# Optimization experiments

Hardware: AMD Instinct MI355X
Metric: run time of the kernel (lower is better)

## Reference

```python
import jax, jax.numpy as jnp
import numpy as np

N, E, FDIM, HID, HEADS, C, L, G = 50000, 800000, 512, 256, 8, 32, 3, 64
EPS = 1e-5


def setup_inputs() -> dict:
    key = jax.random.key(0)
    ks = jax.random.split(key, 16)
    x = jax.random.normal(ks[0], (N, FDIM), dtype=jnp.float32)
    edge_index = jax.random.randint(ks[1], (2, E), 0, N, dtype=jnp.int32)
    batch = jnp.sort(jax.random.randint(ks[2], (N,), 0, G, dtype=jnp.int32))
    s = lambda f: 1.0 / np.sqrt(f)
    return {
        "x": x,
        "edge_index": edge_index,
        "batch": batch,
        "in_w": jax.random.normal(ks[3], (FDIM, HID), jnp.float32) * s(FDIM),
        "in_b": jnp.zeros((HID,), jnp.float32),
        "gat_w": jax.random.normal(ks[4], (L, HID, HID), jnp.float32) * s(HID),
        "att_src": jax.random.normal(ks[5], (L, HEADS, C), jnp.float32) * s(C),
        "att_dst": jax.random.normal(ks[6], (L, HEADS, C), jnp.float32) * s(C),
        "gat_b": jnp.zeros((L, HID), jnp.float32),
        "res_w": jax.random.normal(ks[7], (L, HID, HID), jnp.float32) * s(HID),
        "res_b": jnp.zeros((L, HID), jnp.float32),
        "ln_g": jnp.ones((L, HID), jnp.float32),
        "ln_b": jnp.zeros((L, HID), jnp.float32),
        "pool_w": jax.random.normal(ks[8], (2 * HID, HID), jnp.float32) * s(2 * HID),
        "pool_b": jnp.zeros((HID,), jnp.float32),
    }


def _gat_layer(h, src, dst, w, a_src, a_dst, b):
    # PyG GATConv, concat=True, negative_slope=0.2, dropout inactive (eval)
    xh = (h @ w).reshape(N, HEADS, C)                      # [N,H,C]
    asn = jnp.einsum('nhc,hc->nh', xh, a_src)              # [N,H]
    adn = jnp.einsum('nhc,hc->nh', xh, a_dst)
    e = jax.nn.leaky_relu(asn[src] + adn[dst], 0.2)        # [E2,H]
    # scatter-softmax over destination neighborhoods
    m = jax.ops.segment_max(e, dst, num_segments=N)
    m = jnp.where(jnp.isfinite(m), m, 0.0)
    ex = jnp.exp(e - m[dst])
    den = jax.ops.segment_sum(ex, dst, num_segments=N)
    alpha = ex / (den[dst] + 1e-16)                        # [E2,H]
    msg = xh[src] * alpha[:, :, None]                      # [E2,H,C]
    out = jax.ops.segment_sum(msg, dst, num_segments=N)    # [N,H,C]
    return out.reshape(N, HID) + b


def _layer_norm(h, g, b):
    mu = jnp.mean(h, axis=-1, keepdims=True)
    var = jnp.mean((h - mu) ** 2, axis=-1, keepdims=True)
    return (h - mu) * jax.lax.rsqrt(var + EPS) * g + b


def reference(x, edge_index, batch, in_w, in_b, gat_w, att_src, att_dst, gat_b,
              res_w, res_b, ln_g, ln_b, pool_w, pool_b):
    loops = jnp.arange(N, dtype=edge_index.dtype)          # GATConv add_self_loops=True
    src = jnp.concatenate([edge_index[0], loops])
    dst = jnp.concatenate([edge_index[1], loops])
    h = x @ in_w + in_b
    for i in range(L):
        h_res = h @ res_w[i] + res_b[i]
        h = _gat_layer(h, src, dst, gat_w[i], att_src[i], att_dst[i], gat_b[i])
        h = jax.nn.relu(_layer_norm(h + h_res, ln_g[i], ln_b[i]))
    ones = jnp.ones((N,), h.dtype)
    cnt = jax.ops.segment_sum(ones, batch, num_segments=G)
    h_mean = jax.ops.segment_sum(h, batch, num_segments=G) / jnp.maximum(cnt, 1.0)[:, None]
    h_max = jax.ops.segment_max(h, batch, num_segments=G)
    h_cat = jnp.concatenate([h_mean, h_max], axis=1)       # [G, 2*HID]
    return jax.nn.relu(h_cat @ pool_w + pool_b)            # [G, HID]
```

## Files before the change

kernel.cpp:

```cpp
#include <hip/hip_runtime.h>
#include <math.h>

#define N_NODES 50000
#define E_EDGES 800000
#define E2 (E_EDGES + N_NODES)
#define M_PAD 50048
#define FDIM 512
#define HID 256
#define HEADS 8
#define CDIM 32
#define LAYERS 3
#define GRAPHS 64
#define LN_EPS 1e-5f
#define POOL_P 16

typedef unsigned short ushort_t;
typedef __attribute__((ext_vector_type(8))) short short8v;
typedef __attribute__((ext_vector_type(4))) float f32x4;

__device__ __forceinline__ float bf2f(ushort_t u) {
    union { unsigned int i; float f; } v;
    v.i = ((unsigned int)u) << 16;
    return v.f;
}
__device__ __forceinline__ ushort_t f2bf(float f) {
    union { float f; unsigned int u; } v;
    v.f = f;
    unsigned int r = (v.u + 0x7FFFu + ((v.u >> 16) & 1u)) >> 16;
    return (ushort_t)r;
}
__device__ __forceinline__ void gload_lds16(const void* g, void* l) {
    __builtin_amdgcn_global_load_lds(
        (const __attribute__((address_space(1))) void*)g,
        (__attribute__((address_space(3))) void*)l, 16, 0, 0);
}

__global__ void k_count(const int* __restrict__ ei, int* __restrict__ cnt) {
    int e = blockIdx.x * 256 + threadIdx.x;
    if (e >= E2) return;
    int dst = (e < E_EDGES) ? ei[E_EDGES + e] : (e - E_EDGES);
    atomicAdd(&cnt[dst], 1);
}

__global__ void k_scan1(const int* __restrict__ cnt, int* __restrict__ part) {
    __shared__ int s[256];
    int t = threadIdx.x;
    int i = blockIdx.x * 256 + t;
    s[t] = (i < N_NODES) ? cnt[i] : 0;
    __syncthreads();
    for (int d = 128; d > 0; d >>= 1) {
        if (t < d) s[t] += s[t + d];
        __syncthreads();
    }
    if (t == 0) part[blockIdx.x] = s[0];
}

__global__ void k_scan2(int* __restrict__ part, int nb, int* __restrict__ rowptr) {
    __shared__ int s[256];
    int t = threadIdx.x;
    int v = (t < nb) ? part[t] : 0;
    s[t] = v;
    __syncthreads();
    for (int d = 1; d < 256; d <<= 1) {
        int x = (t >= d) ? s[t - d] : 0;
        __syncthreads();
        s[t] += x;
        __syncthreads();
    }
    if (t < nb) part[t] = s[t] - v;
    if (t == 255) rowptr[N_NODES] = s[255];
}

__global__ void k_scan3(const int* __restrict__ cnt, const int* __restrict__ part,
                        int* __restrict__ rowptr) {
    __shared__ int s[256];
    int t = threadIdx.x;
    int i = blockIdx.x * 256 + t;
    int v = (i < N_NODES) ? cnt[i] : 0;
    s[t] = v;
    __syncthreads();
    for (int d = 1; d < 256; d <<= 1) {
        int x = (t >= d) ? s[t - d] : 0;
        __syncthreads();
        s[t] += x;
        __syncthreads();
    }
    if (i < N_NODES) rowptr[i] = part[blockIdx.x] + s[t] - v;
}

__global__ void k_fill(const int* __restrict__ ei, const int* __restrict__ rowptr,
                       int* __restrict__ fill, int* __restrict__ colv) {
    int e = blockIdx.x * 256 + threadIdx.x;
    if (e >= E2) return;
    int src, dst;
    if (e < E_EDGES) { src = ei[e]; dst = ei[E_EDGES + e]; }
    else             { src = dst = e - E_EDGES; }
    int pos = atomicAdd(&fill[dst], 1);
    colv[rowptr[dst] + pos] = src;
}

__global__ void k_bounds(const int* __restrict__ batch, int* __restrict__ rowstart) {
    int n = blockIdx.x * 256 + threadIdx.x;
    if (n >= N_NODES) return;
    int b = batch[n];
    int bp = (n == 0) ? -1 : batch[n - 1];
    for (int g = bp + 1; g <= b; ++g) rowstart[g] = n;
    if (n == N_NODES - 1) {
        for (int g = b + 1; g <= GRAPHS; ++g) rowstart[g] = N_NODES;
    }
}

__global__ __launch_bounds__(256) void k_cast_x(const float* __restrict__ x,
                                                ushort_t* __restrict__ xb) {
    long long i8 = ((long long)blockIdx.x * 256 + threadIdx.x) * 8;
    if (i8 >= (long long)M_PAD * FDIM) return;
    int row = (int)(i8 >> 9);
    ushort_t o[8];
    if (row < N_NODES) {
        const float* p = x + i8;
        #pragma unroll
        for (int j = 0; j < 8; ++j) o[j] = f2bf(p[j]);
    } else {
        #pragma unroll
        for (int j = 0; j < 8; ++j) o[j] = 0;
    }
    *(short8v*)(xb + i8) = *(short8v*)o;
}

#define IN_ELEMS (FDIM * HID)
#define MAT_ELEMS (HID * HID)
#define WT_TOTAL (IN_ELEMS + 2 * LAYERS * MAT_ELEMS)
__global__ __launch_bounds__(256) void k_wtrans_all(const float* __restrict__ in_w,
                                                    const float* __restrict__ gat_w,
                                                    const float* __restrict__ res_w,
                                                    ushort_t* __restrict__ wt_in,
                                                    ushort_t* __restrict__ wt2) {
    int id = blockIdx.x * 256 + threadIdx.x;
    if (id >= WT_TOTAL) return;
    if (id < IN_ELEMS) {
        int k = id >> 8, n = id & 255;
        wt_in[(size_t)n * FDIM + k] = f2bf(in_w[id]);
    } else {
        int r = id - IN_ELEMS;
        int mat = r >> 16;
        int layer = mat >> 1;
        int isgat = mat & 1;
        int within = r & 65535;
        int k = within >> 8, n = within & 255;
        const float* W = (isgat ? gat_w : res_w) + (size_t)layer * MAT_ELEMS;
        wt2[(size_t)layer * 512 * HID + (size_t)(isgat * 256 + n) * HID + k] =
            f2bf(W[within]);
    }
}

template<int K>
__global__ __launch_bounds__(256) void k_gemm_bf16(const ushort_t* __restrict__ A,
                                                   const ushort_t* __restrict__ BT,
                                                   const float* __restrict__ bias0,
                                                   const float* __restrict__ bias1,
                                                   ushort_t* __restrict__ C0,
                                                   ushort_t* __restrict__ C1, int M) {
    __shared__ char lds[16384] __attribute__((aligned(16)));
    const int bm = blockIdx.x * 128;
    const int bn = blockIdx.y * 128;
    const int t = threadIdx.x, w = t >> 6, l = t & 63;
    const int wr = w >> 1, wc = w & 1;

    const int c1 = t, c2 = t + 256;
    const int ar1 = c1 >> 2, as1 = (c1 & 3) ^ ((ar1 >> 1) & 3);
    const int ar2 = c2 >> 2, as2 = (c2 & 3) ^ ((ar2 >> 1) & 3);
    const ushort_t* pa1 = A + (size_t)(bm + ar1) * K + as1 * 8;
    const ushort_t* pa2 = A + (size_t)(bm + ar2) * K + as2 * 8;
    const ushort_t* pb1 = BT + (size_t)(bn + ar1) * K + as1 * 8;
    const ushort_t* pb2 = BT + (size_t)(bn + ar2) * K + as2 * 8;
    char* la1 = lds + w * 1024;
    char* la2 = lds + 4096 + w * 1024;
    char* lb1 = lds + 8192 + w * 1024;
    char* lb2 = lds + 12288 + w * 1024;

    int aoff[4], boff[4];
    const int kb = l >> 4;
    #pragma unroll
    for (int mi = 0; mi < 4; ++mi) {
        int r = wr * 64 + mi * 16 + (l & 15);
        aoff[mi] = r * 64 + ((kb ^ ((r >> 1) & 3)) << 4);
        int c = wc * 64 + mi * 16 + (l & 15);
        boff[mi] = 8192 + c * 64 + ((kb ^ ((c >> 1) & 3)) << 4);
    }

    f32x4 acc[4][4] = {};
    for (int k0 = 0; k0 < K; k0 += 32) {
        gload_lds16(pa1 + k0, la1);
        gload_lds16(pa2 + k0, la2);
        gload_lds16(pb1 + k0, lb1);
        gload_lds16(pb2 + k0, lb2);
        __syncthreads();
        short8v a[4], b[4];
        #pragma unroll
        for (int mi = 0; mi < 4; ++mi) a[mi] = *(const short8v*)(lds + aoff[mi]);
        #pragma unroll
        for (int ni = 0; ni < 4; ++ni) b[ni] = *(const short8v*)(lds + boff[ni]);
        #pragma unroll
        for (int mi = 0; mi < 4; ++mi)
            #pragma unroll
            for (int ni = 0; ni < 4; ++ni)
                acc[mi][ni] = __builtin_amdgcn_mfma_f32_16x16x32_bf16(
                    a[mi], b[ni], acc[mi][ni], 0, 0, 0);
        __syncthreads();
    }

    ushort_t* C = (bn < 256) ? C0 : C1;
    const float* bias = (bn < 256) ? bias0 : bias1;
    const int cb = (bn < 256) ? bn : bn - 256;
    #pragma unroll
    for (int mi = 0; mi < 4; ++mi) {
        int row = bm + wr * 64 + mi * 16 + (l >> 4) * 4;
        #pragma unroll
        for (int ni = 0; ni < 4; ++ni) {
            int col = cb + wc * 64 + ni * 16 + (l & 15);
            float bv = bias ? bias[col] : 0.f;
            #pragma unroll
            for (int r = 0; r < 4; ++r) {
                if (row + r < M)
                    C[(size_t)(row + r) * HID + col] = f2bf(acc[mi][ni][r] + bv);
            }
        }
    }
}

__global__ __launch_bounds__(256) void k_scores(const ushort_t* __restrict__ xhb,
                                                const float* __restrict__ a_src,
                                                const float* __restrict__ a_dst,
                                                float* __restrict__ asn,
                                                float* __restrict__ adn) {
    int wave = threadIdx.x >> 6, lane = threadIdx.x & 63;
    int n = blockIdx.x * 4 + wave;
    if (n >= N_NODES) return;
    int head = lane >> 3, part = lane & 7;
    ushort4 u = *(const ushort4*)(xhb + (size_t)n * HID + head * CDIM + part * 4);
    float vx = bf2f(u.x), vy = bf2f(u.y), vz = bf2f(u.z), vw = bf2f(u.w);
    const float4 ws = *(const float4*)(a_src + head * CDIM + part * 4);
    const float4 wd = *(const float4*)(a_dst + head * CDIM + part * 4);
    float ds_ = vx * ws.x + vy * ws.y + vz * ws.z + vw * ws.w;
    float dd_ = vx * wd.x + vy * wd.y + vz * wd.z + vw * wd.w;
    for (int d = 1; d < 8; d <<= 1) {
        ds_ += __shfl_xor(ds_, d);
        dd_ += __shfl_xor(dd_, d);
    }
    if (part == 0) {
        asn[n * HEADS + head] = ds_;
        adn[n * HEADS + head] = dd_;
    }
}

__global__ __launch_bounds__(256) void k_agg_ln(const ushort_t* __restrict__ xhb,
                                                const float* __restrict__ asn,
                                                const float* __restrict__ adn,
                                                const int* __restrict__ rowptr,
                                                const int* __restrict__ colv,
                                                const ushort_t* __restrict__ hresb,
                                                const float* __restrict__ gb,
                                                const float* __restrict__ g,
                                                const float* __restrict__ b,
                                                ushort_t* __restrict__ hb) {
    const int wave = threadIdx.x >> 6, lane = threadIdx.x & 63;
    const int n = blockIdx.x * 4 + wave;
    if (n >= N_NODES) return;
    const int half = lane >> 5;
    const int lh = lane & 31;
    const int head = lh >> 2;
    const int ch0 = lh * 8;
    const float adn_h = adn[n * HEADS + head];
    const int j0 = rowptr[n], j1 = rowptr[n + 1];

    float acc[8] = {};
    float den = 0.f;
    int base = j0;
    for (; base + 8 <= j1; base += 8) {
        int idx[4];
        #pragma unroll
        for (int q = 0; q < 4; ++q) idx[q] = colv[base + 2 * q + half];
        short8v u[4];
        #pragma unroll
        for (int q = 0; q < 4; ++q)
            u[q] = *(const short8v*)(xhb + (size_t)idx[q] * HID + ch0);
        float p[4];
        #pragma unroll
        for (int q = 0; q < 4; ++q) {
            float e = asn[idx[q] * HEADS + head] + adn_h;
            e = (e > 0.f) ? e : 0.2f * e;
            p[q] = __expf(e);
        }
        #pragma unroll
        for (int q = 0; q < 4; ++q) {
            den += p[q];
            #pragma unroll
            for (int c = 0; c < 8; ++c)
                acc[c] += p[q] * bf2f((ushort_t)u[q][c]);
        }
    }
    for (; base < j1; base += 2) {
        bool valid = (base + half) < j1;
        int s = valid ? colv[base + half] : n;
        short8v u = *(const short8v*)(xhb + (size_t)s * HID + ch0);
        float e = asn[s * HEADS + head] + adn_h;
        e = (e > 0.f) ? e : 0.2f * e;
        float p = valid ? __expf(e) : 0.f;
        den += p;
        #pragma unroll
        for (int c = 0; c < 8; ++c)
            acc[c] += p * bf2f((ushort_t)u[c]);
    }
    den += __shfl_xor(den, 32);
    #pragma unroll
    for (int c = 0; c < 8; ++c) acc[c] += __shfl_xor(acc[c], 32);

    const float inv = 1.f / (den + 1e-16f);
    short8v hr = *(const short8v*)(hresb + (size_t)n * HID + ch0);
    float4 gbA = *(const float4*)(gb + ch0);
    float4 gbB = *(const float4*)(gb + ch0 + 4);
    float v[8];
    #pragma unroll
    for (int c = 0; c < 8; ++c) {
        float gbv = (c < 4) ? ((const float*)&gbA)[c] : ((const float*)&gbB)[c - 4];
        v[c] = acc[c] * inv + bf2f((ushort_t)hr[c]) + gbv;
    }
    float s = 0.f;
    #pragma unroll
    for (int c = 0; c < 8; ++c) s += v[c];
    #pragma unroll
    for (int d = 1; d < 32; d <<= 1) s += __shfl_xor(s, d);
    const float mu = s * (1.f / HID);
    float q = 0.f;
    #pragma unroll
    for (int c = 0; c < 8; ++c) {
        v[c] -= mu;
        q += v[c] * v[c];
    }
    #pragma unroll
    for (int d = 1; d < 32; d <<= 1) q += __shfl_xor(q, d);
    const float rstd = rsqrtf(q * (1.f / HID) + LN_EPS);
    float4 gA = *(const float4*)(g + ch0);
    float4 gB = *(const float4*)(g + ch0 + 4);
    float4 bA = *(const float4*)(b + ch0);
    float4 bB = *(const float4*)(b + ch0 + 4);
    ushort_t o[8];
    #pragma unroll
    for (int c = 0; c < 8; ++c) {
        float gv = (c < 4) ? ((const float*)&gA)[c] : ((const float*)&gB)[c - 4];
        float bv = (c < 4) ? ((const float*)&bA)[c] : ((const float*)&bB)[c - 4];
        o[c] = f2bf(fmaxf(v[c] * rstd * gv + bv, 0.f));
    }
    if (half == 0)
        *(short8v*)(hb + (size_t)n * HID + ch0) = *(short8v*)o;
}

__global__ __launch_bounds__(256) void k_pool1(const ushort_t* __restrict__ hb,
                                               const int* __restrict__ rowstart,
                                               float* __restrict__ part) {
    int g = blockIdx.x, p = blockIdx.y, c = threadIdx.x;
    int s0 = rowstart[g], s1 = rowstart[g + 1];
    float sum = 0.f, mx = -INFINITY;
    for (int n = s0 + p; n < s1; n += POOL_P) {
        float v = bf2f(hb[(size_t)n * HID + c]);
        sum += v;
        mx = fmaxf(mx, v);
    }
    float* pp = part + (size_t)(g * POOL_P + p) * 512;
    pp[c] = sum;
    pp[256 + c] = mx;
}

__global__ __launch_bounds__(256) void k_pool2(const float* __restrict__ part,
                                               const int* __restrict__ rowstart,
                                               float* __restrict__ hcat) {
    int g = blockIdx.x, c = threadIdx.x;
    float sum = 0.f, mx = -INFINITY;
    for (int p = 0; p < POOL_P; ++p) {
        const float* pp = part + (size_t)(g * POOL_P + p) * 512;
        sum += pp[c];
        mx = fmaxf(mx, pp[256 + c]);
    }
    float cntf = (float)(rowstart[g + 1] - rowstart[g]);
    hcat[(size_t)g * (2 * HID) + c] = sum / fmaxf(cntf, 1.f);
    hcat[(size_t)g * (2 * HID) + HID + c] = mx;
}

__global__ __launch_bounds__(256) void k_pool_gemm(const float* __restrict__ hcat,
                                                   const float* __restrict__ W,
                                                   const float* __restrict__ bias,
                                                   float* __restrict__ out) {
    int g = blockIdx.x, c = threadIdx.x;
    const float* hg = hcat + (size_t)g * (2 * HID);
    float acc = bias[c];
    for (int k = 0; k < 2 * HID; ++k)
        acc += hg[k] * W[(size_t)k * HID + c];
    out[(size_t)g * HID + c] = fmaxf(acc, 0.f);
}

extern "C" void kernel_launch(void* const* d_in, const int* in_sizes, int n_in,
                              void* d_out, int out_size, void* d_ws, size_t ws_size,
                              hipStream_t stream) {
    const float* x       = (const float*)d_in[0];
    const int*   ei      = (const int*)d_in[1];
    const int*   batch   = (const int*)d_in[2];
    const float* in_w    = (const float*)d_in[3];
    const float* in_b    = (const float*)d_in[4];
    const float* gat_w   = (const float*)d_in[5];
    const float* att_src = (const float*)d_in[6];
    const float* att_dst = (const float*)d_in[7];
    const float* gat_b   = (const float*)d_in[8];
    const float* res_w   = (const float*)d_in[9];
    const float* res_b   = (const float*)d_in[10];
    const float* ln_g    = (const float*)d_in[11];
    const float* ln_b    = (const float*)d_in[12];
    const float* pool_w  = (const float*)d_in[13];
    const float* pool_b  = (const float*)d_in[14];
    float* out = (float*)d_out;

    char* ws = (char*)d_ws;
    size_t off = 0;
    auto alloc = [&](size_t bytes) -> char* {
        char* p = ws + off;
        off = (off + bytes + 255) & ~(size_t)255;
        return p;
    };
    ushort_t* xb    = (ushort_t*)alloc((size_t)M_PAD * FDIM * 2);
    ushort_t* hb    = (ushort_t*)alloc((size_t)M_PAD * HID * 2);
    ushort_t* xhb   = (ushort_t*)alloc((size_t)M_PAD * HID * 2);
    ushort_t* hresb = (ushort_t*)alloc((size_t)M_PAD * HID * 2);
    float* asn      = (float*)alloc((size_t)N_NODES * HEADS * 4);
    float* adn      = (float*)alloc((size_t)N_NODES * HEADS * 4);
    int*   cnt      = (int*)alloc((size_t)N_NODES * 4);
    int*   fill     = (int*)alloc((size_t)N_NODES * 4);
    int*   rowptr   = (int*)alloc((size_t)(N_NODES + 1) * 4);
    int*   colv     = (int*)alloc((size_t)E2 * 4);
    int*   part     = (int*)alloc(256 * 4);
    int*   rowstart = (int*)alloc((size_t)(GRAPHS + 1) * 4);
    ushort_t* wt_in = (ushort_t*)alloc((size_t)HID * FDIM * 2);
    ushort_t* wt2   = (ushort_t*)alloc((size_t)LAYERS * 512 * HID * 2);
    float* poolpart = (float*)alloc((size_t)GRAPHS * POOL_P * 512 * 4);
    float* hcat     = (float*)alloc((size_t)GRAPHS * 2 * HID * 4);

    hipMemsetAsync(cnt, 0, (size_t)N_NODES * 4, stream);
    hipMemsetAsync(fill, 0, (size_t)N_NODES * 4, stream);

    const int ge = (E2 + 255) / 256;
    const int nb = (N_NODES + 255) / 256;
    k_count<<<ge, 256, 0, stream>>>(ei, cnt);
    k_scan1<<<nb, 256, 0, stream>>>(cnt, part);
    k_scan2<<<1, 256, 0, stream>>>(part, nb, rowptr);
    k_scan3<<<nb, 256, 0, stream>>>(cnt, part, rowptr);
    k_fill<<<ge, 256, 0, stream>>>(ei, rowptr, fill, colv);
    k_bounds<<<nb, 256, 0, stream>>>(batch, rowstart);

    k_cast_x<<<(int)(((size_t)M_PAD * FDIM / 8 + 255) / 256), 256, 0, stream>>>(x, xb);
    k_wtrans_all<<<(WT_TOTAL + 255) / 256, 256, 0, stream>>>(in_w, gat_w, res_w,
                                                             wt_in, wt2);

    dim3 gg1(M_PAD / 128, 2);
    k_gemm_bf16<FDIM><<<gg1, 256, 0, stream>>>(xb, wt_in, in_b, nullptr,
                                               hb, nullptr, N_NODES);

    const int nw = (N_NODES + 3) / 4;
    dim3 gg2(M_PAD / 128, 4);
    for (int i = 0; i < LAYERS; ++i) {
        k_gemm_bf16<HID><<<gg2, 256, 0, stream>>>(hb, wt2 + (size_t)i * 512 * HID,
                                                  res_b + (size_t)i * HID, nullptr,
                                                  hresb, xhb, N_NODES);
        k_scores<<<nw, 256, 0, stream>>>(xhb, att_src + (size_t)i * HEADS * CDIM,
                                         att_dst + (size_t)i * HEADS * CDIM, asn, adn);
        k_agg_ln<<<nw, 256, 0, stream>>>(xhb, asn, adn, rowptr, colv, hresb,
                                         gat_b + (size_t)i * HID,
                                         ln_g + (size_t)i * HID,
                                         ln_b + (size_t)i * HID, hb);
    }
    dim3 pg(GRAPHS, POOL_P);
    k_pool1<<<pg, 256, 0, stream>>>(hb, rowstart, poolpart);
    k_pool2<<<GRAPHS, 256, 0, stream>>>(poolpart, rowstart, hcat);
    k_pool_gemm<<<GRAPHS, 256, 0, stream>>>(hcat, pool_w, pool_b, out);
}
```

Measured before the change: 587.5 us.

## Double-buffer GEMM LDS, fuse attention scores into GEMM epilogue, merge pool kernels

The bf16 GEMM now double-buffers its LDS tiles and prefetches the next K slice before waiting on the current one, with explicit vmcnt waits and raw barriers. The per-node attention score dot products are computed in the GEMM epilogue from the fp32 accumulators using shuffle reductions, which removes the separate k_scores kernel and its re-read of xh. The pool reduction and the final pool GEMM are merged into one kernel through shared memory. This doubles LDS use per block, which may lower occupancy, and the scores are now computed from fp32 values rather than from bf16-rounded ones, so they can differ slightly.

```diff
diff --git a/kernel.cpp b/kernel.cpp
--- a/kernel.cpp
+++ b/kernel.cpp
@@ -157,10 +157,14 @@
 __global__ __launch_bounds__(256) void k_gemm_bf16(const ushort_t* __restrict__ A,
                                                    const ushort_t* __restrict__ BT,
                                                    const float* __restrict__ bias0,
-                                                   const float* __restrict__ bias1,
                                                    ushort_t* __restrict__ C0,
-                                                   ushort_t* __restrict__ C1, int M) {
-    __shared__ char lds[16384] __attribute__((aligned(16)));
+                                                   ushort_t* __restrict__ C1,
+                                                   const float* __restrict__ a_src,
+                                                   const float* __restrict__ a_dst,
+                                                   float* __restrict__ asn,
+                                                   float* __restrict__ adn, int M) {
+    __shared__ char lds[32768] __attribute__((aligned(16)));
+    constexpr int NT = K / 32;
     const int bm = blockIdx.x * 128;
     const int bn = blockIdx.y * 128;
     const int t = threadIdx.x, w = t >> 6, l = t & 63;
@@ -173,10 +177,6 @@
     const ushort_t* pa2 = A + (size_t)(bm + ar2) * K + as2 * 8;
     const ushort_t* pb1 = BT + (size_t)(bn + ar1) * K + as1 * 8;
     const ushort_t* pb2 = BT + (size_t)(bn + ar2) * K + as2 * 8;
-    char* la1 = lds + w * 1024;
-    char* la2 = lds + 4096 + w * 1024;
-    char* lb1 = lds + 8192 + w * 1024;
-    char* lb2 = lds + 12288 + w * 1024;
 
     int aoff[4], boff[4];
     const int kb = l >> 4;
@@ -188,29 +188,42 @@
         boff[mi] = 8192 + c * 64 + ((kb ^ ((c >> 1) & 3)) << 4);
     }
 
+    auto STAGE = [&](int buf, int k0) {
+        char* base = lds + buf * 16384;
+        gload_lds16(pa1 + k0, base + w * 1024);
+        gload_lds16(pa2 + k0, base + 4096 + w * 1024);
+        gload_lds16(pb1 + k0, base + 8192 + w * 1024);
+        gload_lds16(pb2 + k0, base + 12288 + w * 1024);
+    };
+
+    STAGE(0, 0);
     f32x4 acc[4][4] = {};
-    for (int k0 = 0; k0 < K; k0 += 32) {
-        gload_lds16(pa1 + k0, la1);
-        gload_lds16(pa2 + k0, la2);
-        gload_lds16(pb1 + k0, lb1);
-        gload_lds16(pb2 + k0, lb2);
-        __syncthreads();
+    #pragma unroll
+    for (int tt = 0; tt < NT; ++tt) {
+        if (tt + 1 < NT) {
+            STAGE((tt + 1) & 1, (tt + 1) * 32);
+            asm volatile("s_waitcnt vmcnt(4)" ::: "memory");
+        } else {
+            asm volatile("s_waitcnt vmcnt(0)" ::: "memory");
+        }
+        __builtin_amdgcn_s_barrier();
+        const char* base = lds + (tt & 1) * 16384;
         short8v a[4], b[4];
         #pragma unroll
-        for (int mi = 0; mi < 4; ++mi) a[mi] = *(const short8v*)(lds + aoff[mi]);
-        #pragma unroll
-        for (int ni = 0; ni < 4; ++ni) b[ni] = *(const short8v*)(lds + boff[ni]);
+        for (int mi = 0; mi < 4; ++mi) a[mi] = *(const short8v*)(base + aoff[mi]);
+        #pragma unroll
+        for (int ni = 0; ni < 4; ++ni) b[ni] = *(const short8v*)(base + boff[ni]);
         #pragma unroll
         for (int mi = 0; mi < 4; ++mi)
             #pragma unroll
             for (int ni = 0; ni < 4; ++ni)
                 acc[mi][ni] = __builtin_amdgcn_mfma_f32_16x16x32_bf16(
                     a[mi], b[ni], acc[mi][ni], 0, 0, 0);
-        __syncthreads();
+        __builtin_amdgcn_s_barrier();
     }
 
     ushort_t* C = (bn < 256) ? C0 : C1;
-    const float* bias = (bn < 256) ? bias0 : bias1;
+    const float* bias = (bn < 256) ? bias0 : nullptr;
     const int cb = (bn < 256) ? bn : bn - 256;
     #pragma unroll
     for (int mi = 0; mi < 4; ++mi) {
@@ -226,30 +239,44 @@
             }
         }
     }
-}
-
-__global__ __launch_bounds__(256) void k_scores(const ushort_t* __restrict__ xhb,
-                                                const float* __restrict__ a_src,
-                                                const float* __restrict__ a_dst,
-                                                float* __restrict__ asn,
-                                                float* __restrict__ adn) {
-    int wave = threadIdx.x >> 6, lane = threadIdx.x & 63;
-    int n = blockIdx.x * 4 + wave;
-    if (n >= N_NODES) return;
-    int head = lane >> 3, part = lane & 7;
-    ushort4 u = *(const ushort4*)(xhb + (size_t)n * HID + head * CDIM + part * 4);
-    float vx = bf2f(u.x), vy = bf2f(u.y), vz = bf2f(u.z), vw = bf2f(u.w);
-    const float4 ws = *(const float4*)(a_src + head * CDIM + part * 4);
-    const float4 wd = *(const float4*)(a_dst + head * CDIM + part * 4);
-    float ds_ = vx * ws.x + vy * ws.y + vz * ws.z + vw * ws.w;
-    float dd_ = vx * wd.x + vy * wd.y + vz * wd.z + vw * wd.w;
-    for (int d = 1; d < 8; d <<= 1) {
-        ds_ += __shfl_xor(ds_, d);
-        dd_ += __shfl_xor(dd_, d);
-    }
-    if (part == 0) {
-        asn[n * HEADS + head] = ds_;
-        adn[n * HEADS + head] = dd_;
+
+    if (asn && bn >= 256) {
+        const int cbase = bn - 256;
+        #pragma unroll
+        for (int mi = 0; mi < 4; ++mi) {
+            int row = bm + wr * 64 + mi * 16 + (l >> 4) * 4;
+            #pragma unroll
+            for (int p = 0; p < 2; ++p) {
+                int c0 = cbase + wc * 64 + (2 * p) * 16 + (l & 15);
+                int c1c = c0 + 16;
+                int head = c0 >> 5;
+                float as0 = a_src[c0], as1 = a_src[c1c];
+                float ad0 = a_dst[c0], ad1 = a_dst[c1c];
+                float vs[4], vd[4];
+                #pragma unroll
+                for (int r = 0; r < 4; ++r) {
+                    vs[r] = acc[mi][2 * p][r] * as0 + acc[mi][2 * p + 1][r] * as1;
+                    vd[r] = acc[mi][2 * p][r] * ad0 + acc[mi][2 * p + 1][r] * ad1;
+                }
+                #pragma unroll
+                for (int d = 1; d < 16; d <<= 1) {
+                    #pragma unroll
+                    for (int r = 0; r < 4; ++r) {
+                        vs[r] += __shfl_xor(vs[r], d);
+                        vd[r] += __shfl_xor(vd[r], d);
+                    }
+                }
+                if ((l & 15) == 0) {
+                    #pragma unroll
+                    for (int r = 0; r < 4; ++r) {
+                        if (row + r < N_NODES) {
+                            asn[(row + r) * HEADS + head] = vs[r];
+                            adn[(row + r) * HEADS + head] = vd[r];
+                        }
+                    }
+                }
+            }
+        }
     }
 }
 
@@ -371,9 +398,12 @@
     pp[256 + c] = mx;
 }
 
-__global__ __launch_bounds__(256) void k_pool2(const float* __restrict__ part,
-                                               const int* __restrict__ rowstart,
-                                               float* __restrict__ hcat) {
+__global__ __launch_bounds__(256) void k_pool2g(const float* __restrict__ part,
+                                                const int* __restrict__ rowstart,
+                                                const float* __restrict__ W,
+                                                const float* __restrict__ bias,
+                                                float* __restrict__ out) {
+    __shared__ float hc[512];
     int g = blockIdx.x, c = threadIdx.x;
     float sum = 0.f, mx = -INFINITY;
     for (int p = 0; p < POOL_P; ++p) {
@@ -382,19 +412,13 @@
         mx = fmaxf(mx, pp[256 + c]);
     }
     float cntf = (float)(rowstart[g + 1] - rowstart[g]);
-    hcat[(size_t)g * (2 * HID) + c] = sum / fmaxf(cntf, 1.f);
-    hcat[(size_t)g * (2 * HID) + HID + c] = mx;
-}
-
-__global__ __launch_bounds__(256) void k_pool_gemm(const float* __restrict__ hcat,
-                                                   const float* __restrict__ W,
-                                                   const float* __restrict__ bias,
-                                                   float* __restrict__ out) {
-    int g = blockIdx.x, c = threadIdx.x;
-    const float* hg = hcat + (size_t)g * (2 * HID);
+    hc[c] = sum / fmaxf(cntf, 1.f);
+    hc[256 + c] = mx;
+    __syncthreads();
     float acc = bias[c];
+    #pragma unroll 8
     for (int k = 0; k < 2 * HID; ++k)
-        acc += hg[k] * W[(size_t)k * HID + c];
+        acc += hc[k] * W[(size_t)k * HID + c];
     out[(size_t)g * HID + c] = fmaxf(acc, 0.f);
 }
 
@@ -440,7 +464,6 @@
     ushort_t* wt_in = (ushort_t*)alloc((size_t)HID * FDIM * 2);
     ushort_t* wt2   = (ushort_t*)alloc((size_t)LAYERS * 512 * HID * 2);
     float* poolpart = (float*)alloc((size_t)GRAPHS * POOL_P * 512 * 4);
-    float* hcat     = (float*)alloc((size_t)GRAPHS * 2 * HID * 4);
 
     hipMemsetAsync(cnt, 0, (size_t)N_NODES * 4, stream);
     hipMemsetAsync(fill, 0, (size_t)N_NODES * 4, stream);
@@ -459,17 +482,19 @@
                                                              wt_in, wt2);
 
     dim3 gg1(M_PAD / 128, 2);
-    k_gemm_bf16<FDIM><<<gg1, 256, 0, stream>>>(xb, wt_in, in_b, nullptr,
-                                               hb, nullptr, N_NODES);
+    k_gemm_bf16<FDIM><<<gg1, 256, 0, stream>>>(xb, wt_in, in_b, hb, nullptr,
+                                               nullptr, nullptr, nullptr, nullptr,
+                                               N_NODES);
 
     const int nw = (N_NODES + 3) / 4;
     dim3 gg2(M_PAD / 128, 4);
     for (int i = 0; i < LAYERS; ++i) {
         k_gemm_bf16<HID><<<gg2, 256, 0, stream>>>(hb, wt2 + (size_t)i * 512 * HID,
-                                                  res_b + (size_t)i * HID, nullptr,
-                                                  hresb, xhb, N_NODES);
-        k_scores<<<nw, 256, 0, stream>>>(xhb, att_src + (size_t)i * HEADS * CDIM,
-                                         att_dst + (size_t)i * HEADS * CDIM, asn, adn);
+                                                  res_b + (size_t)i * HID,
+                                                  hresb, xhb,
+                                                  att_src + (size_t)i * HEADS * CDIM,
+                                                  att_dst + (size_t)i * HEADS * CDIM,
+                                                  asn, adn, N_NODES);
         k_agg_ln<<<nw, 256, 0, stream>>>(xhb, asn, adn, rowptr, colv, hresb,
                                          gat_b + (size_t)i * HID,
                                          ln_g + (size_t)i * HID,
@@ -477,6 +502,5 @@
     }
     dim3 pg(GRAPHS, POOL_P);
     k_pool1<<<pg, 256, 0, stream>>>(hb, rowstart, poolpart);
-    k_pool2<<<GRAPHS, 256, 0, stream>>>(poolpart, rowstart, hcat);
-    k_pool_gemm<<<GRAPHS, 256, 0, stream>>>(hcat, pool_w, pool_b, out);
-}
+    k_pool2g<<<GRAPHS, 256, 0, stream>>>(poolpart, rowstart, pool_w, pool_b, out);
+}
```

Measured after the change: 625.4 us. 6.4% more time.
